# Optimization experiments

Measured on AMD Instinct MI355X. Metric: run time of the kernel, lower is better.

The kernel has to match this reference:

```python
import jax, jax.numpy as jnp
import numpy as np

B, N, C = 32, 128, 128
HE = 64                      # n_hidden_edge
FILTERS = [64, 256, 512]
K = 3
NREL = 2
NH = 256                     # n_hidden
OUT = 10
EPS_BN = 1e-5


def _lin(key, fin, fout):
    return jax.random.normal(key, (fin, fout), jnp.float32) / np.sqrt(fin)


def setup_inputs() -> dict:
    key = jax.random.key(0)
    ks = iter(jax.random.split(key, 64))
    x = jax.random.normal(next(ks), (B, N, C), jnp.float32)
    # ragged mask: first n_b nodes active
    n_nodes = jax.random.randint(next(ks), (B,), 64, N + 1)
    mask = (jnp.arange(N)[None, :] < n_nodes[:, None]).astype(jnp.float32)
    A = jax.random.uniform(next(ks), (B, N, N), jnp.float32)
    A = A * mask[:, :, None] * mask[:, None, :]
    inp = {"x": x, "A": A, "mask": mask}
    # edge predictor MLP: Linear(2C,HE) -> ReLU -> Linear(HE,1)
    inp["eW1"] = _lin(next(ks), 2 * C, HE)
    inp["eb1"] = jnp.zeros((HE,), jnp.float32)
    inp["eW2"] = _lin(next(ks), HE, 1)
    inp["eb2"] = jnp.zeros((1,), jnp.float32)
    # 3 GraphConv layers: fc (in*K*NREL -> f), BN eval params
    fin = C
    for li, f in enumerate(FILTERS):
        inp[f"gW{li}"] = _lin(next(ks), fin * K * NREL, f)
        inp[f"gb{li}"] = jnp.zeros((f,), jnp.float32)
        inp[f"g{li}g"] = jnp.ones((f,), jnp.float32)
        inp[f"g{li}b"] = jnp.zeros((f,), jnp.float32)
        inp[f"g{li}m"] = 0.1 * jax.random.normal(next(ks), (f,), jnp.float32)
        inp[f"g{li}v"] = jax.random.uniform(next(ks), (f,), jnp.float32) + 0.5
        fin = f
    # classifier fc (dropout is identity in eval)
    inp["fW1"] = _lin(next(ks), FILTERS[-1], NH)
    inp["fb1"] = jnp.zeros((NH,), jnp.float32)
    inp["fW2"] = _lin(next(ks), NH, OUT)
    inp["fb2"] = jnp.zeros((OUT,), jnp.float32)
    return inp


def _edge_adjacency(x, mask, eW1, eb1, eW2, eb2):
    # edge_pred(cat(x_i,x_j)) for all pairs; flipped pass == transpose of scores
    u = x @ eW1[:C]          # [B,N,HE] (contribution of node i slot)
    v = x @ eW1[C:]          # [B,N,HE] (contribution of node j slot)
    h = jax.nn.relu(u[:, :, None, :] + v[:, None, :, :] + eb1)   # [B,N,N,HE]
    s = jnp.einsum('bijh,h->bij', h, eW2[:, 0]) + eb2[0]          # [B,N,N]
    y = jnp.exp(0.5 * (s + jnp.swapaxes(s, 1, 2)))
    # only masked upper-triangular pairs (i<j) were scattered in the original
    tri = jnp.triu(jnp.ones((N, N), bool), 1)
    pm = tri[None, :, :] * (mask[:, :, None] * mask[:, None, :])
    A_pred = y * pm
    rs = jnp.sum(A_pred, axis=2)                                 # row sums (torch sum over dim 1 of [N,N])
    rs = jnp.where(rs == 0.0, 1.0, rs)
    An = A_pred / rs[:, :, None]
    return An + jnp.swapaxes(An, 1, 2)


def _gconv(xh, A2, mask, W, b, g, be, m, v):
    outs = []
    for rel in range(A2.shape[-1]):
        Ar = A2[..., rel]
        # K>=2, scale_identity=False -> no identity added
        D = (jnp.sum(Ar, axis=1) + 1e-5) ** (-0.5)               # [B,N]
        L = D[:, :, None] * Ar * D[:, None, :]
        Xt = [xh, jnp.matmul(L, xh)]
        for _ in range(2, K):
            Xt.append(2.0 * jnp.matmul(L, Xt[-1]) - Xt[-2])
        outs.append(jnp.concatenate(Xt, axis=2))
    h = jnp.concatenate(outs, axis=2) @ W + b
    h = h * mask[:, :, None]
    h = (h - m) / jnp.sqrt(v + EPS_BN) * g + be                  # BatchNorm1d eval over channel dim
    return jax.nn.relu(h)


def reference(x, A, mask, eW1, eb1, eW2, eb2,
              gW0, gb0, g0g, g0b, g0m, g0v,
              gW1, gb1, g1g, g1b, g1m, g1v,
              gW2, gb2, g2g, g2b, g2m, g2v,
              fW1, fb1, fW2, fb2):
    An = _edge_adjacency(x, mask, eW1, eb1, eW2, eb2)
    A2 = jnp.stack((A, An), axis=3)                              # [B,N,N,2]
    h = _gconv(x, A2, mask, gW0, gb0, g0g, g0b, g0m, g0v)
    h = _gconv(h, A2, mask, gW1, gb1, g1g, g1b, g1m, g1v)
    h = _gconv(h, A2, mask, gW2, gb2, g2g, g2b, g2m, g2v)
    pooled = jnp.max(h, axis=1)                                  # [B, 512]
    # fc: Dropout(eval=id) -> Linear -> Dropout(eval=id) -> Linear (no activation)
    return (pooled @ fW1 + fb1) @ fW2 + fb2
```

## Files before the change

kernel.cpp:

```cpp
#include <hip/hip_runtime.h>

#define Bk 32
#define Nn 128
#define Cc 128
#define HE 64
#define BN_EPS 1e-5f

typedef __attribute__((ext_vector_type(8))) short short8;
typedef __attribute__((ext_vector_type(4))) float floatx4;

#define OFF_UV   ((size_t)0)
#define OFF_AP   ((size_t)524288)
#define OFF_LB   ((size_t)1048576)
#define OFF_H0   ((size_t)1572864)
#define OFF_H1   ((size_t)1835008)
#define OFF_WC   ((size_t)2899968)
#define OFF_BC   ((size_t)2905088)
#define OFF_XB0  ((size_t)2905104)
#define OFF_XB   ((size_t)3167248)
#define OFF_WT   ((size_t)6312976)
#define WUV_OFS  933888

__device__ __forceinline__ unsigned short f2b(float f) {
    unsigned int x = __float_as_uint(f);
    unsigned int r = x + 0x7FFFu + ((x >> 16) & 1u);
    return (unsigned short)(r >> 16);
}

__global__ __launch_bounds__(256) void prep_all(const float* __restrict__ W0,
                                                const float* __restrict__ W1,
                                                const float* __restrict__ W2,
                                                const float* __restrict__ eW1,
                                                const float* __restrict__ fW1,
                                                const float* __restrict__ fb1,
                                                const float* __restrict__ fW2,
                                                const float* __restrict__ fb2,
                                                const float* __restrict__ x,
                                                unsigned short* __restrict__ Wt,
                                                float* __restrict__ Wc,
                                                float* __restrict__ bc,
                                                unsigned short* __restrict__ xb0) {
    __shared__ unsigned short Ts[64][65];
    int bid = blockIdx.x, tid = threadIdx.x;
    if (bid < 228) {
        const float* src; unsigned short* dst; int N, ldK, k0, n0;
        if (bid < 12)      { src = W0; dst = Wt;          N = 64;  ldK = 768;  k0 = bid * 64;        n0 = 0; }
        else if (bid < 36) { int t = bid - 12; src = W1; dst = Wt + 49152;  N = 256; ldK = 384;  k0 = (t % 6) * 64;  n0 = (t / 6) * 64; }
        else               { int t = bid - 36; src = W2; dst = Wt + 147456; N = 512; ldK = 1536; k0 = (t % 24) * 64; n0 = (t / 24) * 64; }
#pragma unroll
        for (int p = 0; p < 16; ++p) {
            int e = tid + p * 256; int r = e >> 6, c = e & 63;
            Ts[r][c] = f2b(src[(size_t)(k0 + r) * N + n0 + c]);
        }
        __syncthreads();
#pragma unroll
        for (int p = 0; p < 16; ++p) {
            int e = tid + p * 256; int n = e >> 6, k = e & 63;
            dst[(size_t)(n0 + n) * ldK + k0 + k] = Ts[k][n];
        }
        return;
    }
    if (bid < 232) {
        int tt = bid - 228;
        int half = tt >> 1, kt = tt & 1;
        int k0 = kt * 64;
        unsigned short* Wuv = Wt + WUV_OFS;
#pragma unroll
        for (int p = 0; p < 16; ++p) {
            int e = tid + p * 256; int r = e >> 6, c = e & 63;
            Ts[r][c] = f2b(eW1[(size_t)(half * 128 + k0 + r) * 64 + c]);
        }
        __syncthreads();
#pragma unroll
        for (int p = 0; p < 16; ++p) {
            int e = tid + p * 256; int n = e >> 6, k = e & 63;
            Wuv[(size_t)(half * 64 + n) * 128 + k0 + k] = Ts[k][n];
        }
        return;
    }
    if (bid < 253) {
        int e = (bid - 232) * 256 + tid;
        if (e < 5120) {
            int i = e / 10, j = e - i * 10;
            float acc = 0.f;
            for (int h = 0; h < 256; ++h) acc += fW1[(size_t)i * 256 + h] * fW2[(size_t)h * 10 + j];
            Wc[e] = acc;
        } else if (e < 5130) {
            int j = e - 5120;
            float acc = fb2[j];
            for (int h = 0; h < 256; ++h) acc += fb1[h] * fW2[(size_t)h * 10 + j];
            bc[j] = acc;
        }
        return;
    }
    {
        int idx = (bid - 253) * 256 + tid;
        float4 vv = ((const float4*)x)[idx];
        ushort4 o;
        o.x = f2b(vv.x); o.y = f2b(vv.y); o.z = f2b(vv.z); o.w = f2b(vv.w);
        ((ushort4*)xb0)[idx] = o;
    }
}

__global__ __launch_bounds__(256) void uv_mfma(const unsigned short* __restrict__ xb0,
                                               const unsigned short* __restrict__ Wuv,
                                               const float* __restrict__ eb1,
                                               float* __restrict__ uv) {
    __shared__ __align__(16) unsigned short As[128 * 40];
    __shared__ __align__(16) unsigned short Bs[64 * 40];
    int tid = threadIdx.x;
    int w = tid >> 6, lane = tid & 63, quad = lane >> 4, lr = lane & 15;
    int row0 = blockIdx.y * 128, col0 = blockIdx.x * 64;
    floatx4 acc[2][4];
#pragma unroll
    for (int rt = 0; rt < 2; ++rt)
#pragma unroll
        for (int ct = 0; ct < 4; ++ct) acc[rt][ct] = (floatx4){0.f, 0.f, 0.f, 0.f};
    int arow[2], asub[2];
#pragma unroll
    for (int i = 0; i < 2; ++i) { int ch = tid + i * 256; arow[i] = ch >> 2; asub[i] = ch & 3; }
    int brow = tid >> 2, bsub = tid & 3;
    for (int k0 = 0; k0 < 128; k0 += 32) {
        short8 ra[2];
#pragma unroll
        for (int i = 0; i < 2; ++i)
            ra[i] = *(const short8*)(xb0 + (size_t)(row0 + arow[i]) * 128 + k0 + asub[i] * 8);
        short8 rb = *(const short8*)(Wuv + (size_t)(col0 + brow) * 128 + k0 + bsub * 8);
        __syncthreads();
#pragma unroll
        for (int i = 0; i < 2; ++i) *(short8*)&As[arow[i] * 40 + asub[i] * 8] = ra[i];
        *(short8*)&Bs[brow * 40 + bsub * 8] = rb;
        __syncthreads();
        short8 a[2], b[4];
#pragma unroll
        for (int rt = 0; rt < 2; ++rt)
            a[rt] = *(const short8*)&As[(w * 32 + rt * 16 + lr) * 40 + quad * 8];
#pragma unroll
        for (int ct = 0; ct < 4; ++ct)
            b[ct] = *(const short8*)&Bs[(ct * 16 + lr) * 40 + quad * 8];
#pragma unroll
        for (int rt = 0; rt < 2; ++rt)
#pragma unroll
            for (int ct = 0; ct < 4; ++ct)
                acc[rt][ct] = __builtin_amdgcn_mfma_f32_16x16x32_bf16(a[rt], b[ct], acc[rt][ct], 0, 0, 0);
    }
#pragma unroll
    for (int rt = 0; rt < 2; ++rt) {
        int rbase = row0 + w * 32 + rt * 16 + quad * 4;
#pragma unroll
        for (int ct = 0; ct < 4; ++ct) {
            int col = col0 + ct * 16 + lr;
            float bi = (col < 64) ? eb1[col] : 0.f;
#pragma unroll
            for (int reg = 0; reg < 4; ++reg)
                uv[(size_t)(rbase + reg) * 128 + col] = acc[rt][ct][reg] + bi;
        }
    }
}

__global__ __launch_bounds__(256) void edge_sym(const float* __restrict__ uv,
                                                const float* __restrict__ eW2,
                                                const float* __restrict__ eb2,
                                                const float* __restrict__ mask,
                                                float* __restrict__ ap) {
    __shared__ __align__(16) float ui[16][68], vi[16][68], uj[16][68], vj[16][68];
    __shared__ __align__(16) float w2[64];
    int t = blockIdx.x, b = blockIdx.y;
    int ti = 0, rem = t;
    for (;;) { int w = 8 - ti; if (rem < w) break; rem -= w; ++ti; }
    int tj = ti + rem;
    int i0 = ti * 16, j0 = tj * 16;
    int tid = threadIdx.x;
    int r = tid >> 4, c4 = (tid & 15) * 4;
    const float* uvb = uv + (size_t)b * Nn * 128;
    *(float4*)&ui[r][c4] = *(const float4*)(uvb + (size_t)(i0 + r) * 128 + c4);
    *(float4*)&vi[r][c4] = *(const float4*)(uvb + (size_t)(i0 + r) * 128 + 64 + c4);
    *(float4*)&uj[r][c4] = *(const float4*)(uvb + (size_t)(j0 + r) * 128 + c4);
    *(float4*)&vj[r][c4] = *(const float4*)(uvb + (size_t)(j0 + r) * 128 + 64 + c4);
    if (tid < 64) w2[tid] = eW2[tid];
    __syncthreads();
    int il = tid >> 4, jl = tid & 15;
    int gi = i0 + il, gj = j0 + jl;
    if (gj <= gi) return;
    float d = 0.f;
#pragma unroll
    for (int h4 = 0; h4 < 16; ++h4) {
        float4 a1 = *(const float4*)&ui[il][h4 * 4];
        float4 b1 = *(const float4*)&vj[jl][h4 * 4];
        float4 a2 = *(const float4*)&uj[jl][h4 * 4];
        float4 b2 = *(const float4*)&vi[il][h4 * 4];
        float4 ww = *(const float4*)&w2[h4 * 4];
        d += (fmaxf(a1.x + b1.x, 0.f) + fmaxf(a2.x + b2.x, 0.f)) * ww.x
           + (fmaxf(a1.y + b1.y, 0.f) + fmaxf(a2.y + b2.y, 0.f)) * ww.y
           + (fmaxf(a1.z + b1.z, 0.f) + fmaxf(a2.z + b2.z, 0.f)) * ww.z
           + (fmaxf(a1.w + b1.w, 0.f) + fmaxf(a2.w + b2.w, 0.f)) * ww.w;
    }
    float p = 0.5f * d + eb2[0];
    float mi = mask[b * Nn + gi], mj = mask[b * Nn + gj];
    float val = (mi != 0.f && mj != 0.f) ? expf(fminf(p, 80.f)) : 0.f;
    ap[((size_t)(b * Nn + gi)) * Nn + gj] = val;
}

__global__ __launch_bounds__(256) void adj_L(const float* __restrict__ ap,
                                             const float* __restrict__ A,
                                             unsigned short* __restrict__ Lb) {
    int bid = blockIdx.x, tid = threadIdx.x;
    if (bid < 32) {
        int b = bid;
        __shared__ float apS[128][129];
        __shared__ float part[256], invS[128], t1S[128], Dv[128];
        const float* apg = ap + (size_t)b * Nn * Nn;
        for (int k = 0; k < 64; ++k) {
            int idx = tid + k * 256;
            int i = idx >> 7, j = idx & 127;
            float g = apg[idx];
            apS[i][j] = (j > i) ? g : 0.f;
        }
        __syncthreads();
        {
            int row = tid >> 1, half = tid & 1;
            float s0 = 0.f;
            for (int j = half * 64; j < half * 64 + 64; ++j) s0 += apS[row][j];
            part[tid] = s0;
        }
        __syncthreads();
        if (tid < 128) {
            float rsum = part[tid * 2] + part[tid * 2 + 1];
            invS[tid] = (rsum == 0.f) ? 1.f : (1.f / rsum);
            t1S[tid]  = (rsum == 0.f) ? 0.f : 1.f;
        }
        __syncthreads();
        {
            int col = tid >> 1, half = tid & 1;
            float s0 = 0.f;
            for (int j = half * 64; j < half * 64 + 64; ++j) s0 += apS[j][col] * invS[j];
            part[tid] = s0;
        }
        __syncthreads();
        if (tid < 128) Dv[tid] = rsqrtf(t1S[tid] + part[tid * 2] + part[tid * 2 + 1] + 1e-5f);
        __syncthreads();
        unsigned short* Lo = Lb + ((size_t)(Bk + b)) * Nn * Nn;
        for (int k = 0; k < 64; ++k) {
            int idx = tid + k * 256;
            int i = idx >> 7, j = idx & 127;
            float an = apS[i][j] * invS[i] + apS[j][i] * invS[j];
            Lo[idx] = f2b(Dv[i] * an * Dv[j]);
        }
    } else {
        int b = bid - 32;
        const float* Ar = A + (size_t)b * Nn * Nn;
        __shared__ float part2[256];
        __shared__ float Ds[128];
        int j = tid & 127, half = tid >> 7;
        float sum = 0.f;
        for (int i = half * 64; i < half * 64 + 64; ++i) sum += Ar[i * Nn + j];
        part2[tid] = sum;
        __syncthreads();
        if (tid < 128) Ds[tid] = rsqrtf(part2[tid] + part2[tid + 128] + 1e-5f);
        __syncthreads();
        unsigned short* Lo = Lb + (size_t)b * Nn * Nn;
        for (int k = 0; k < 64; ++k) {
            int idx = tid + k * 256;
            int i = idx >> 7, jj = idx & 127;
            Lo[idx] = f2b(Ds[i] * Ar[idx] * Ds[jj]);
        }
    }
}

template <int FIN>
__global__ __launch_bounds__(256) void cheb_v4(const unsigned short* __restrict__ Lb,
                                               const float* __restrict__ xin,
                                               unsigned short* __restrict__ Xb) {
    constexpr int LDK = 136;
    __shared__ __align__(16) unsigned short XsT[32 * LDK];
    __shared__ __align__(16) unsigned short T1T[32 * LDK];
    int z = blockIdx.y;
    int b = z & 31, rel = z >> 5;
    int c0 = blockIdx.x * 32;
    int tid = threadIdx.x;
    int w = tid >> 6, lane = tid & 63, quad = lane >> 4, lr = lane & 15;
    const unsigned short* Lp = Lb + ((size_t)(rel * Bk + b)) * Nn * Nn;
    const float* Xp = xin + (size_t)b * Nn * FIN;
    const int ld6 = 6 * FIN;
    unsigned short* Xo = Xb + (size_t)b * Nn * ld6 + rel * 3 * FIN;

    short8 aL[2][4];
#pragma unroll
    for (int rt = 0; rt < 2; ++rt) {
        int row = w * 32 + rt * 16 + lr;
#pragma unroll
        for (int kc = 0; kc < 4; ++kc)
            aL[rt][kc] = *(const short8*)(Lp + (size_t)row * Nn + kc * 32 + quad * 8);
    }
    {
        int node = tid >> 1, cb = (tid & 1) * 16;
        const float* xr = Xp + (size_t)node * FIN + c0 + cb;
        unsigned short* t0w = Xo + (size_t)node * ld6 + c0 + cb;
#pragma unroll
        for (int i = 0; i < 4; ++i) {
            float4 vv = *(const float4*)(xr + i * 4);
            ushort4 o;
            o.x = f2b(vv.x); o.y = f2b(vv.y); o.z = f2b(vv.z); o.w = f2b(vv.w);
            *(ushort4*)(t0w + i * 4) = o;
            XsT[(cb + i * 4 + 0) * LDK + node] = o.x;
            XsT[(cb + i * 4 + 1) * LDK + node] = o.y;
            XsT[(cb + i * 4 + 2) * LDK + node] = o.z;
            XsT[(cb + i * 4 + 3) * LDK + node] = o.w;
        }
    }
    __syncthreads();

    floatx4 acc1[2][2];
#pragma unroll
    for (int rt = 0; rt < 2; ++rt)
#pragma unroll
        for (int ct = 0; ct < 2; ++ct) acc1[rt][ct] = (floatx4){0.f, 0.f, 0.f, 0.f};
#pragma unroll
    for (int kc = 0; kc < 4; ++kc) {
        short8 bb[2];
#pragma unroll
        for (int ct = 0; ct < 2; ++ct)
            bb[ct] = *(const short8*)&XsT[(ct * 16 + lr) * LDK + kc * 32 + quad * 8];
#pragma unroll
        for (int rt = 0; rt < 2; ++rt)
#pragma unroll
            for (int ct = 0; ct < 2; ++ct)
                acc1[rt][ct] = __builtin_amdgcn_mfma_f32_16x16x32_bf16(aL[rt][kc], bb[ct], acc1[rt][ct], 0, 0, 0);
    }
#pragma unroll
    for (int rt = 0; rt < 2; ++rt) {
        int rb = (w * 2 + rt) * 16 + quad * 4;
#pragma unroll
        for (int ct = 0; ct < 2; ++ct) {
            int col = ct * 16 + lr;
            ushort4 o;
            o.x = f2b(acc1[rt][ct][0]); o.y = f2b(acc1[rt][ct][1]);
            o.z = f2b(acc1[rt][ct][2]); o.w = f2b(acc1[rt][ct][3]);
            *(ushort4*)&T1T[col * LDK + rb] = o;
        }
    }
    __syncthreads();

    {
        int node = tid >> 1, cb = (tid & 1) * 16;
        unsigned short* t1w = Xo + (size_t)node * ld6 + FIN + c0 + cb;
#pragma unroll
        for (int i = 0; i < 4; ++i) {
            ushort4 o;
            o.x = T1T[(cb + i * 4 + 0) * LDK + node];
            o.y = T1T[(cb + i * 4 + 1) * LDK + node];
            o.z = T1T[(cb + i * 4 + 2) * LDK + node];
            o.w = T1T[(cb + i * 4 + 3) * LDK + node];
            *(ushort4*)(t1w + i * 4) = o;
        }
    }
    floatx4 acc2[2][2];
#pragma unroll
    for (int rt = 0; rt < 2; ++rt)
#pragma unroll
        for (int ct = 0; ct < 2; ++ct) acc2[rt][ct] = (floatx4){0.f, 0.f, 0.f, 0.f};
#pragma unroll
    for (int kc = 0; kc < 4; ++kc) {
        short8 bb[2];
#pragma unroll
        for (int ct = 0; ct < 2; ++ct)
            bb[ct] = *(const short8*)&T1T[(ct * 16 + lr) * LDK + kc * 32 + quad * 8];
#pragma unroll
        for (int rt = 0; rt < 2; ++rt)
#pragma unroll
            for (int ct = 0; ct < 2; ++ct)
                acc2[rt][ct] = __builtin_amdgcn_mfma_f32_16x16x32_bf16(aL[rt][kc], bb[ct], acc2[rt][ct], 0, 0, 0);
    }
#pragma unroll
    for (int rt = 0; rt < 2; ++rt) {
        int rb = (w * 2 + rt) * 16 + quad * 4;
#pragma unroll
        for (int ct = 0; ct < 2; ++ct) {
            int col = ct * 16 + lr;
            ushort4 o;
            float t0a = Xp[(size_t)(rb + 0) * FIN + c0 + col];
            float t0b = Xp[(size_t)(rb + 1) * FIN + c0 + col];
            float t0c = Xp[(size_t)(rb + 2) * FIN + c0 + col];
            float t0d = Xp[(size_t)(rb + 3) * FIN + c0 + col];
            o.x = f2b(2.f * acc2[rt][ct][0] - t0a);
            o.y = f2b(2.f * acc2[rt][ct][1] - t0b);
            o.z = f2b(2.f * acc2[rt][ct][2] - t0c);
            o.w = f2b(2.f * acc2[rt][ct][3] - t0d);
            *(ushort4*)&XsT[col * LDK + rb] = o;
        }
    }
    __syncthreads();
    {
        int node = tid >> 1, cb = (tid & 1) * 16;
        unsigned short* t2w = Xo + (size_t)node * ld6 + 2 * FIN + c0 + cb;
#pragma unroll
        for (int i = 0; i < 4; ++i) {
            ushort4 o;
            o.x = XsT[(cb + i * 4 + 0) * LDK + node];
            o.y = XsT[(cb + i * 4 + 1) * LDK + node];
            o.z = XsT[(cb + i * 4 + 2) * LDK + node];
            o.w = XsT[(cb + i * 4 + 3) * LDK + node];
            *(ushort4*)(t2w + i * 4) = o;
        }
    }
}

template <int RT, bool POOL>
__global__ __launch_bounds__(256) void fc_mfma(const unsigned short* __restrict__ Xb,
                                               const unsigned short* __restrict__ Wt,
                                               const float* __restrict__ bias,
                                               const float* __restrict__ mask,
                                               const float* __restrict__ bnG,
                                               const float* __restrict__ bnB,
                                               const float* __restrict__ bnM,
                                               const float* __restrict__ bnV,
                                               float* __restrict__ out,
                                               const float* __restrict__ Wc,
                                               const float* __restrict__ bc,
                                               float* __restrict__ outc,
                                               int Kd, int F) {
    __shared__ __align__(16) unsigned short As[RT * 64 * 40];
    __shared__ __align__(16) unsigned short Bs[64 * 40];
    __shared__ float wmax[4][64];
    int tid = threadIdx.x;
    int w = tid >> 6, lane = tid & 63, quad = lane >> 4, lr = lane & 15;
    int row0 = blockIdx.y * (RT * 64), col0 = blockIdx.x * 64;

    floatx4 acc[RT][4];
#pragma unroll
    for (int rt = 0; rt < RT; ++rt)
#pragma unroll
        for (int ct = 0; ct < 4; ++ct) acc[rt][ct] = (floatx4){0.f, 0.f, 0.f, 0.f};

    int arow[RT], asub[RT];
#pragma unroll
    for (int i = 0; i < RT; ++i) { int ch = tid + i * 256; arow[i] = ch >> 2; asub[i] = ch & 3; }
    int brow = tid >> 2, bsub = tid & 3;

    for (int k0 = 0; k0 < Kd; k0 += 32) {
        short8 ra[RT];
#pragma unroll
        for (int i = 0; i < RT; ++i)
            ra[i] = *(const short8*)(Xb + (size_t)(row0 + arow[i]) * Kd + k0 + asub[i] * 8);
        short8 rb = *(const short8*)(Wt + (size_t)(col0 + brow) * Kd + k0 + bsub * 8);
        __syncthreads();
#pragma unroll
        for (int i = 0; i < RT; ++i)
            *(short8*)&As[arow[i] * 40 + asub[i] * 8] = ra[i];
        *(short8*)&Bs[brow * 40 + bsub * 8] = rb;
        __syncthreads();
        short8 a[RT], b[4];
#pragma unroll
        for (int rt = 0; rt < RT; ++rt)
            a[rt] = *(const short8*)&As[(w * RT * 16 + rt * 16 + lr) * 40 + quad * 8];
#pragma unroll
        for (int ct = 0; ct < 4; ++ct)
            b[ct] = *(const short8*)&Bs[(ct * 16 + lr) * 40 + quad * 8];
#pragma unroll
        for (int rt = 0; rt < RT; ++rt)
#pragma unroll
            for (int ct = 0; ct < 4; ++ct)
                acc[rt][ct] = __builtin_amdgcn_mfma_f32_16x16x32_bf16(a[rt], b[ct], acc[rt][ct], 0, 0, 0);
    }

    float cm[4] = {0.f, 0.f, 0.f, 0.f};
#pragma unroll
    for (int rt = 0; rt < RT; ++rt) {
        int rbase = row0 + w * RT * 16 + rt * 16 + quad * 4;
#pragma unroll
        for (int ct = 0; ct < 4; ++ct) {
            int col = col0 + ct * 16 + lr;
            float bi = bias[col];
            float sc = rsqrtf(bnV[col] + BN_EPS) * bnG[col];
            float bm = bnM[col], bb = bnB[col];
#pragma unroll
            for (int reg = 0; reg < 4; ++reg) {
                int row = rbase + reg;
                float h = acc[rt][ct][reg] + bi;
                h *= mask[row];
                h = (h - bm) * sc + bb;
                h = fmaxf(h, 0.f);
                if (POOL) cm[ct] = fmaxf(cm[ct], h);
                else      out[(size_t)row * F + col] = h;
            }
        }
    }
    if (POOL) {
#pragma unroll
        for (int ct = 0; ct < 4; ++ct) {
            cm[ct] = fmaxf(cm[ct], __shfl_xor(cm[ct], 16));
            cm[ct] = fmaxf(cm[ct], __shfl_xor(cm[ct], 32));
            if (quad == 0) wmax[w][ct * 16 + lr] = cm[ct];
        }
        __syncthreads();
        if (tid < 64) {
            float g = fmaxf(fmaxf(wmax[0][tid], wmax[1][tid]), fmaxf(wmax[2][tid], wmax[3][tid]));
            float s[10];
#pragma unroll
            for (int o = 0; o < 10; ++o) s[o] = g * Wc[(size_t)(col0 + tid) * 10 + o];
#pragma unroll
            for (int ofs = 32; ofs > 0; ofs >>= 1)
#pragma unroll
                for (int o = 0; o < 10; ++o) s[o] += __shfl_down(s[o], ofs);
            if (tid == 0) {
                int b = blockIdx.y;
#pragma unroll
                for (int o = 0; o < 10; ++o) {
                    float v = s[o] + ((blockIdx.x == 0) ? bc[o] : 0.f);
                    atomicAdd(&outc[b * 10 + o], v);
                }
            }
        }
    }
}

extern "C" void kernel_launch(void* const* d_in, const int* in_sizes, int n_in,
                              void* d_out, int out_size, void* d_ws, size_t ws_size,
                              hipStream_t stream) {
    const float* x    = (const float*)d_in[0];
    const float* Ain  = (const float*)d_in[1];
    const float* mask = (const float*)d_in[2];
    const float* eW1  = (const float*)d_in[3];
    const float* eb1  = (const float*)d_in[4];
    const float* eW2  = (const float*)d_in[5];
    const float* eb2  = (const float*)d_in[6];
    const float* fW1  = (const float*)d_in[25];
    const float* fb1  = (const float*)d_in[26];
    const float* fW2  = (const float*)d_in[27];
    const float* fb2  = (const float*)d_in[28];

    float* ws = (float*)d_ws;
    float* uv = ws + OFF_UV;
    float* ap = ws + OFF_AP;
    unsigned short* Lb = (unsigned short*)(ws + OFF_LB);
    float* h0 = ws + OFF_H0;
    float* h1 = ws + OFF_H1;
    float* Wc = ws + OFF_WC;
    float* bc = ws + OFF_BC;
    unsigned short* xb0 = (unsigned short*)(ws + OFF_XB0);
    unsigned short* Xb  = (unsigned short*)(ws + OFF_XB);
    unsigned short* Wt  = (unsigned short*)(ws + OFF_WT);

    hipMemsetAsync(d_out, 0, (size_t)out_size * sizeof(float), stream);

    prep_all<<<765, 256, 0, stream>>>((const float*)d_in[7], (const float*)d_in[13],
                                      (const float*)d_in[19], eW1, fW1, fb1, fW2, fb2, x,
                                      Wt, Wc, bc, xb0);

    uv_mfma<<<dim3(2, 32), 256, 0, stream>>>(xb0, Wt + WUV_OFS, eb1, uv);
    edge_sym<<<dim3(36, Bk), 256, 0, stream>>>(uv, eW2, eb2, mask, ap);
    adj_L<<<64, 256, 0, stream>>>(ap, Ain, Lb);

    const float* xins[3] = {x, h0, h1};
    const unsigned short* Wts[3] = {Wt, Wt + 49152, Wt + 147456};
    const int Kds[3] = {768, 384, 1536};
    for (int li = 0; li < 3; ++li) {
        int base = 7 + li * 6;
        const float* gb = (const float*)d_in[base + 1];
        const float* gg = (const float*)d_in[base + 2];
        const float* gB = (const float*)d_in[base + 3];
        const float* gm = (const float*)d_in[base + 4];
        const float* gv = (const float*)d_in[base + 5];

        if (li == 0)      cheb_v4<128><<<dim3(4, 64), 256, 0, stream>>>(Lb, xins[li], Xb);
        else if (li == 1) cheb_v4<64><<<dim3(2, 64), 256, 0, stream>>>(Lb, xins[li], Xb);
        else              cheb_v4<256><<<dim3(8, 64), 256, 0, stream>>>(Lb, xins[li], Xb);

        if (li == 0)
            fc_mfma<1, false><<<dim3(1, 64), 256, 0, stream>>>(
                Xb, Wts[li], gb, mask, gg, gB, gm, gv, h0, nullptr, nullptr, nullptr, Kds[li], 64);
        else if (li == 1)
            fc_mfma<2, false><<<dim3(4, 32), 256, 0, stream>>>(
                Xb, Wts[li], gb, mask, gg, gB, gm, gv, h1, nullptr, nullptr, nullptr, Kds[li], 256);
        else
            fc_mfma<2, true><<<dim3(8, 32), 256, 0, stream>>>(
                Xb, Wts[li], gb, mask, gg, gB, gm, gv, nullptr, Wc, bc, (float*)d_out, Kds[li], 512);
    }
}
```

Before: 235.1 us.

## Fuse all stages into one persistent kernel with grid-wide barriers

Replaces the sequence of separate kernel launches (prep, uv, edge, adjacency, three cheb+fc layers) with a single persistent kernel of 512 blocks that loops over virtual blocks per stage. Stages are separated by a software grid barrier built on global atomics. Independent work is co-scheduled within a stage, such as the A-side adjacency with uv and the first cheb pass with the edge scoring. The adjacency-normalisation stage is split so the A branch runs early, and ap is zeroed in the prep stage. This removes per-launch overhead and tail gaps but adds barrier spin cost. It also depends on all 512 blocks being co-resident, with no cooperative launch guaranteeing that.

```diff
diff --git a/kernel.cpp b/kernel.cpp
--- a/kernel.cpp
+++ b/kernel.cpp
@@ -3,8 +3,8 @@
 #define Bk 32
 #define Nn 128
 #define Cc 128
-#define HE 64
 #define BN_EPS 1e-5f
+#define GRIDN 512
 
 typedef __attribute__((ext_vector_type(8))) short short8;
 typedef __attribute__((ext_vector_type(4))) float floatx4;
@@ -27,90 +27,120 @@
     return (unsigned short)(r >> 16);
 }
 
-__global__ __launch_bounds__(256) void prep_all(const float* __restrict__ W0,
-                                                const float* __restrict__ W1,
-                                                const float* __restrict__ W2,
-                                                const float* __restrict__ eW1,
-                                                const float* __restrict__ fW1,
-                                                const float* __restrict__ fb1,
-                                                const float* __restrict__ fW2,
-                                                const float* __restrict__ fb2,
-                                                const float* __restrict__ x,
-                                                unsigned short* __restrict__ Wt,
-                                                float* __restrict__ Wc,
-                                                float* __restrict__ bc,
-                                                unsigned short* __restrict__ xb0) {
-    __shared__ unsigned short Ts[64][65];
-    int bid = blockIdx.x, tid = threadIdx.x;
-    if (bid < 228) {
+union __align__(16) SMem {
+    struct { unsigned short Ts[64][65]; } prep;
+    struct { unsigned short As[128 * 40]; unsigned short Bs[64 * 40]; } uv;
+    struct { float ui[16][68]; float vi[16][68];
+             float uj[16][68]; float vj[16][68]; float w2[64]; } edge;
+    struct { float part[256]; float invS[128]; float t1S[128]; float Dv[128]; } adj;
+    struct { unsigned short XsT[32 * 136]; unsigned short T1T[32 * 136]; } cheb;
+    struct { unsigned short As[2 * 64 * 40]; unsigned short Bs[64 * 40];
+             float wmax[4][64]; } fc;
+};
+
+__device__ unsigned g_cnt = 0;
+__device__ unsigned g_gen = 0;
+
+__device__ __forceinline__ void gsync() {
+    __syncthreads();
+    if (threadIdx.x == 0) {
+        __threadfence();
+        unsigned gen = __hip_atomic_load(&g_gen, __ATOMIC_RELAXED, __HIP_MEMORY_SCOPE_AGENT);
+        unsigned arr = __hip_atomic_fetch_add(&g_cnt, 1u, __ATOMIC_ACQ_REL, __HIP_MEMORY_SCOPE_AGENT) + 1u;
+        if (arr == (unsigned)GRIDN) {
+            __hip_atomic_store(&g_cnt, 0u, __ATOMIC_RELAXED, __HIP_MEMORY_SCOPE_AGENT);
+            __hip_atomic_fetch_add(&g_gen, 1u, __ATOMIC_ACQ_REL, __HIP_MEMORY_SCOPE_AGENT);
+        } else {
+            while (__hip_atomic_load(&g_gen, __ATOMIC_RELAXED, __HIP_MEMORY_SCOPE_AGENT) == gen)
+                __builtin_amdgcn_s_sleep(2);
+        }
+        __threadfence();
+    }
+    __syncthreads();
+}
+
+struct MArgs {
+    const float *x, *A, *mask, *eW1, *eb1, *eW2, *eb2;
+    const float *W0, *W1, *W2;
+    const float *gb0, *gg0, *gB0, *gm0, *gv0;
+    const float *gb1, *gg1, *gB1, *gm1, *gv1;
+    const float *gb2, *gg2, *gB2, *gm2, *gv2;
+    const float *fW1, *fb1, *fW2, *fb2;
+    float *uv, *ap, *h0, *h1, *Wc, *bc;
+    unsigned short *Lb, *xb0, *Xb, *Wt;
+    float *outc;
+};
+
+__device__ __forceinline__ void st_prep(SMem& sm, int vb, int tid, const MArgs& a) {
+    if (vb < 228) {
         const float* src; unsigned short* dst; int N, ldK, k0, n0;
-        if (bid < 12)      { src = W0; dst = Wt;          N = 64;  ldK = 768;  k0 = bid * 64;        n0 = 0; }
-        else if (bid < 36) { int t = bid - 12; src = W1; dst = Wt + 49152;  N = 256; ldK = 384;  k0 = (t % 6) * 64;  n0 = (t / 6) * 64; }
-        else               { int t = bid - 36; src = W2; dst = Wt + 147456; N = 512; ldK = 1536; k0 = (t % 24) * 64; n0 = (t / 24) * 64; }
+        if (vb < 12)      { src = a.W0; dst = a.Wt;          N = 64;  ldK = 768;  k0 = vb * 64;       n0 = 0; }
+        else if (vb < 36) { int t = vb - 12; src = a.W1; dst = a.Wt + 49152;  N = 256; ldK = 384;  k0 = (t % 6) * 64;  n0 = (t / 6) * 64; }
+        else              { int t = vb - 36; src = a.W2; dst = a.Wt + 147456; N = 512; ldK = 1536; k0 = (t % 24) * 64; n0 = (t / 24) * 64; }
 #pragma unroll
         for (int p = 0; p < 16; ++p) {
             int e = tid + p * 256; int r = e >> 6, c = e & 63;
-            Ts[r][c] = f2b(src[(size_t)(k0 + r) * N + n0 + c]);
+            sm.prep.Ts[r][c] = f2b(src[(size_t)(k0 + r) * N + n0 + c]);
         }
         __syncthreads();
 #pragma unroll
         for (int p = 0; p < 16; ++p) {
             int e = tid + p * 256; int n = e >> 6, k = e & 63;
-            dst[(size_t)(n0 + n) * ldK + k0 + k] = Ts[k][n];
-        }
-        return;
-    }
-    if (bid < 232) {
-        int tt = bid - 228;
+            dst[(size_t)(n0 + n) * ldK + k0 + k] = sm.prep.Ts[k][n];
+        }
+    } else if (vb < 232) {
+        int tt = vb - 228;
         int half = tt >> 1, kt = tt & 1;
         int k0 = kt * 64;
-        unsigned short* Wuv = Wt + WUV_OFS;
+        unsigned short* Wuv = a.Wt + WUV_OFS;
 #pragma unroll
         for (int p = 0; p < 16; ++p) {
             int e = tid + p * 256; int r = e >> 6, c = e & 63;
-            Ts[r][c] = f2b(eW1[(size_t)(half * 128 + k0 + r) * 64 + c]);
+            sm.prep.Ts[r][c] = f2b(a.eW1[(size_t)(half * 128 + k0 + r) * 64 + c]);
         }
         __syncthreads();
 #pragma unroll
         for (int p = 0; p < 16; ++p) {
             int e = tid + p * 256; int n = e >> 6, k = e & 63;
-            Wuv[(size_t)(half * 64 + n) * 128 + k0 + k] = Ts[k][n];
-        }
-        return;
-    }
-    if (bid < 253) {
-        int e = (bid - 232) * 256 + tid;
+            Wuv[(size_t)(half * 64 + n) * 128 + k0 + k] = sm.prep.Ts[k][n];
+        }
+    } else if (vb < 253) {
+        int e = (vb - 232) * 256 + tid;
         if (e < 5120) {
             int i = e / 10, j = e - i * 10;
             float acc = 0.f;
-            for (int h = 0; h < 256; ++h) acc += fW1[(size_t)i * 256 + h] * fW2[(size_t)h * 10 + j];
-            Wc[e] = acc;
+            for (int h = 0; h < 256; ++h) acc += a.fW1[(size_t)i * 256 + h] * a.fW2[(size_t)h * 10 + j];
+            a.Wc[e] = acc;
         } else if (e < 5130) {
             int j = e - 5120;
-            float acc = fb2[j];
-            for (int h = 0; h < 256; ++h) acc += fb1[h] * fW2[(size_t)h * 10 + j];
-            bc[j] = acc;
-        }
-        return;
-    }
-    {
-        int idx = (bid - 253) * 256 + tid;
-        float4 vv = ((const float4*)x)[idx];
+            float acc = a.fb2[j];
+            for (int h = 0; h < 256; ++h) acc += a.fb1[h] * a.fW2[(size_t)h * 10 + j];
+            a.bc[j] = acc;
+        }
+    } else if (vb < 765) {
+        int idx = (vb - 253) * 256 + tid;
+        float4 vv = ((const float4*)a.x)[idx];
         ushort4 o;
         o.x = f2b(vv.x); o.y = f2b(vv.y); o.z = f2b(vv.z); o.w = f2b(vv.w);
-        ((ushort4*)xb0)[idx] = o;
-    }
-}
-
-__global__ __launch_bounds__(256) void uv_mfma(const unsigned short* __restrict__ xb0,
-                                               const unsigned short* __restrict__ Wuv,
-                                               const float* __restrict__ eb1,
-                                               float* __restrict__ uv) {
-    __shared__ __align__(16) unsigned short As[128 * 40];
-    __shared__ __align__(16) unsigned short Bs[64 * 40];
-    int tid = threadIdx.x;
+        ((ushort4*)a.xb0)[idx] = o;
+    } else {
+        int b = vb - 765;
+        float4* dst = (float4*)(a.ap + (size_t)b * Nn * Nn);
+        float4 z4 = {0.f, 0.f, 0.f, 0.f};
+#pragma unroll
+        for (int i = 0; i < 16; ++i) dst[tid + i * 256] = z4;
+    }
+}
+
+__device__ __forceinline__ void st_uv(SMem& sm, int tid, int bx, int by,
+                                      const unsigned short* __restrict__ xb0,
+                                      const unsigned short* __restrict__ Wuv,
+                                      const float* __restrict__ eb1,
+                                      float* __restrict__ uv) {
+    unsigned short* As = sm.uv.As;
+    unsigned short* Bs = sm.uv.Bs;
     int w = tid >> 6, lane = tid & 63, quad = lane >> 4, lr = lane & 15;
-    int row0 = blockIdx.y * 128, col0 = blockIdx.x * 64;
+    int row0 = by * 128, col0 = bx * 64;
     floatx4 acc[2][4];
 #pragma unroll
     for (int rt = 0; rt < 2; ++rt)
@@ -131,18 +161,18 @@
         for (int i = 0; i < 2; ++i) *(short8*)&As[arow[i] * 40 + asub[i] * 8] = ra[i];
         *(short8*)&Bs[brow * 40 + bsub * 8] = rb;
         __syncthreads();
-        short8 a[2], b[4];
+        short8 av[2], bv[4];
 #pragma unroll
         for (int rt = 0; rt < 2; ++rt)
-            a[rt] = *(const short8*)&As[(w * 32 + rt * 16 + lr) * 40 + quad * 8];
+            av[rt] = *(const short8*)&As[(w * 32 + rt * 16 + lr) * 40 + quad * 8];
 #pragma unroll
         for (int ct = 0; ct < 4; ++ct)
-            b[ct] = *(const short8*)&Bs[(ct * 16 + lr) * 40 + quad * 8];
+            bv[ct] = *(const short8*)&Bs[(ct * 16 + lr) * 40 + quad * 8];
 #pragma unroll
         for (int rt = 0; rt < 2; ++rt)
 #pragma unroll
             for (int ct = 0; ct < 4; ++ct)
-                acc[rt][ct] = __builtin_amdgcn_mfma_f32_16x16x32_bf16(a[rt], b[ct], acc[rt][ct], 0, 0, 0);
+                acc[rt][ct] = __builtin_amdgcn_mfma_f32_16x16x32_bf16(av[rt], bv[ct], acc[rt][ct], 0, 0, 0);
     }
 #pragma unroll
     for (int rt = 0; rt < 2; ++rt) {
@@ -158,126 +188,117 @@
     }
 }
 
-__global__ __launch_bounds__(256) void edge_sym(const float* __restrict__ uv,
-                                                const float* __restrict__ eW2,
-                                                const float* __restrict__ eb2,
-                                                const float* __restrict__ mask,
-                                                float* __restrict__ ap) {
-    __shared__ __align__(16) float ui[16][68], vi[16][68], uj[16][68], vj[16][68];
-    __shared__ __align__(16) float w2[64];
-    int t = blockIdx.x, b = blockIdx.y;
+__device__ __forceinline__ void st_adjA(SMem& sm, int tid, int b,
+                                        const float* __restrict__ A,
+                                        unsigned short* __restrict__ Lb) {
+    const float* Ar = A + (size_t)b * Nn * Nn;
+    int j = tid & 127, half = tid >> 7;
+    float sum = 0.f;
+    for (int i = half * 64; i < half * 64 + 64; ++i) sum += Ar[i * Nn + j];
+    sm.adj.part[tid] = sum;
+    __syncthreads();
+    if (tid < 128) sm.adj.Dv[tid] = rsqrtf(sm.adj.part[tid] + sm.adj.part[tid + 128] + 1e-5f);
+    __syncthreads();
+    unsigned short* Lo = Lb + (size_t)b * Nn * Nn;
+    for (int k = 0; k < 64; ++k) {
+        int idx = tid + k * 256;
+        int i = idx >> 7, jj = idx & 127;
+        Lo[idx] = f2b(sm.adj.Dv[i] * Ar[idx] * sm.adj.Dv[jj]);
+    }
+}
+
+__device__ __forceinline__ void st_edge(SMem& sm, int tid, int t, int b,
+                                        const float* __restrict__ uv,
+                                        const float* __restrict__ eW2,
+                                        const float* __restrict__ eb2,
+                                        const float* __restrict__ mask,
+                                        float* __restrict__ ap) {
     int ti = 0, rem = t;
     for (;;) { int w = 8 - ti; if (rem < w) break; rem -= w; ++ti; }
     int tj = ti + rem;
     int i0 = ti * 16, j0 = tj * 16;
-    int tid = threadIdx.x;
     int r = tid >> 4, c4 = (tid & 15) * 4;
     const float* uvb = uv + (size_t)b * Nn * 128;
-    *(float4*)&ui[r][c4] = *(const float4*)(uvb + (size_t)(i0 + r) * 128 + c4);
-    *(float4*)&vi[r][c4] = *(const float4*)(uvb + (size_t)(i0 + r) * 128 + 64 + c4);
-    *(float4*)&uj[r][c4] = *(const float4*)(uvb + (size_t)(j0 + r) * 128 + c4);
-    *(float4*)&vj[r][c4] = *(const float4*)(uvb + (size_t)(j0 + r) * 128 + 64 + c4);
-    if (tid < 64) w2[tid] = eW2[tid];
+    *(float4*)&sm.edge.ui[r][c4] = *(const float4*)(uvb + (size_t)(i0 + r) * 128 + c4);
+    *(float4*)&sm.edge.vi[r][c4] = *(const float4*)(uvb + (size_t)(i0 + r) * 128 + 64 + c4);
+    *(float4*)&sm.edge.uj[r][c4] = *(const float4*)(uvb + (size_t)(j0 + r) * 128 + c4);
+    *(float4*)&sm.edge.vj[r][c4] = *(const float4*)(uvb + (size_t)(j0 + r) * 128 + 64 + c4);
+    if (tid < 64) sm.edge.w2[tid] = eW2[tid];
     __syncthreads();
     int il = tid >> 4, jl = tid & 15;
     int gi = i0 + il, gj = j0 + jl;
-    if (gj <= gi) return;
-    float d = 0.f;
-#pragma unroll
-    for (int h4 = 0; h4 < 16; ++h4) {
-        float4 a1 = *(const float4*)&ui[il][h4 * 4];
-        float4 b1 = *(const float4*)&vj[jl][h4 * 4];
-        float4 a2 = *(const float4*)&uj[jl][h4 * 4];
-        float4 b2 = *(const float4*)&vi[il][h4 * 4];
-        float4 ww = *(const float4*)&w2[h4 * 4];
-        d += (fmaxf(a1.x + b1.x, 0.f) + fmaxf(a2.x + b2.x, 0.f)) * ww.x
-           + (fmaxf(a1.y + b1.y, 0.f) + fmaxf(a2.y + b2.y, 0.f)) * ww.y
-           + (fmaxf(a1.z + b1.z, 0.f) + fmaxf(a2.z + b2.z, 0.f)) * ww.z
-           + (fmaxf(a1.w + b1.w, 0.f) + fmaxf(a2.w + b2.w, 0.f)) * ww.w;
-    }
-    float p = 0.5f * d + eb2[0];
-    float mi = mask[b * Nn + gi], mj = mask[b * Nn + gj];
-    float val = (mi != 0.f && mj != 0.f) ? expf(fminf(p, 80.f)) : 0.f;
-    ap[((size_t)(b * Nn + gi)) * Nn + gj] = val;
-}
-
-__global__ __launch_bounds__(256) void adj_L(const float* __restrict__ ap,
-                                             const float* __restrict__ A,
-                                             unsigned short* __restrict__ Lb) {
-    int bid = blockIdx.x, tid = threadIdx.x;
-    if (bid < 32) {
-        int b = bid;
-        __shared__ float apS[128][129];
-        __shared__ float part[256], invS[128], t1S[128], Dv[128];
-        const float* apg = ap + (size_t)b * Nn * Nn;
-        for (int k = 0; k < 64; ++k) {
-            int idx = tid + k * 256;
-            int i = idx >> 7, j = idx & 127;
-            float g = apg[idx];
-            apS[i][j] = (j > i) ? g : 0.f;
-        }
-        __syncthreads();
-        {
-            int row = tid >> 1, half = tid & 1;
-            float s0 = 0.f;
-            for (int j = half * 64; j < half * 64 + 64; ++j) s0 += apS[row][j];
-            part[tid] = s0;
-        }
-        __syncthreads();
-        if (tid < 128) {
-            float rsum = part[tid * 2] + part[tid * 2 + 1];
-            invS[tid] = (rsum == 0.f) ? 1.f : (1.f / rsum);
-            t1S[tid]  = (rsum == 0.f) ? 0.f : 1.f;
-        }
-        __syncthreads();
-        {
-            int col = tid >> 1, half = tid & 1;
-            float s0 = 0.f;
-            for (int j = half * 64; j < half * 64 + 64; ++j) s0 += apS[j][col] * invS[j];
-            part[tid] = s0;
-        }
-        __syncthreads();
-        if (tid < 128) Dv[tid] = rsqrtf(t1S[tid] + part[tid * 2] + part[tid * 2 + 1] + 1e-5f);
-        __syncthreads();
-        unsigned short* Lo = Lb + ((size_t)(Bk + b)) * Nn * Nn;
-        for (int k = 0; k < 64; ++k) {
-            int idx = tid + k * 256;
-            int i = idx >> 7, j = idx & 127;
-            float an = apS[i][j] * invS[i] + apS[j][i] * invS[j];
-            Lo[idx] = f2b(Dv[i] * an * Dv[j]);
-        }
-    } else {
-        int b = bid - 32;
-        const float* Ar = A + (size_t)b * Nn * Nn;
-        __shared__ float part2[256];
-        __shared__ float Ds[128];
-        int j = tid & 127, half = tid >> 7;
-        float sum = 0.f;
-        for (int i = half * 64; i < half * 64 + 64; ++i) sum += Ar[i * Nn + j];
-        part2[tid] = sum;
-        __syncthreads();
-        if (tid < 128) Ds[tid] = rsqrtf(part2[tid] + part2[tid + 128] + 1e-5f);
-        __syncthreads();
-        unsigned short* Lo = Lb + (size_t)b * Nn * Nn;
-        for (int k = 0; k < 64; ++k) {
-            int idx = tid + k * 256;
-            int i = idx >> 7, jj = idx & 127;
-            Lo[idx] = f2b(Ds[i] * Ar[idx] * Ds[jj]);
-        }
+    if (gj > gi) {
+        float d = 0.f;
+#pragma unroll
+        for (int h4 = 0; h4 < 16; ++h4) {
+            float4 a1 = *(const float4*)&sm.edge.ui[il][h4 * 4];
+            float4 b1 = *(const float4*)&sm.edge.vj[jl][h4 * 4];
+            float4 a2 = *(const float4*)&sm.edge.uj[jl][h4 * 4];
+            float4 b2 = *(const float4*)&sm.edge.vi[il][h4 * 4];
+            float4 ww = *(const float4*)&sm.edge.w2[h4 * 4];
+            d += (fmaxf(a1.x + b1.x, 0.f) + fmaxf(a2.x + b2.x, 0.f)) * ww.x
+               + (fmaxf(a1.y + b1.y, 0.f) + fmaxf(a2.y + b2.y, 0.f)) * ww.y
+               + (fmaxf(a1.z + b1.z, 0.f) + fmaxf(a2.z + b2.z, 0.f)) * ww.z
+               + (fmaxf(a1.w + b1.w, 0.f) + fmaxf(a2.w + b2.w, 0.f)) * ww.w;
+        }
+        float p = 0.5f * d + eb2[0];
+        float mi = mask[b * Nn + gi], mj = mask[b * Nn + gj];
+        float val = (mi != 0.f && mj != 0.f) ? expf(fminf(p, 80.f)) : 0.f;
+        ap[((size_t)(b * Nn + gi)) * Nn + gj] = val;
+    }
+}
+
+__device__ __forceinline__ void st_adjAn(SMem& sm, int tid, int b,
+                                         const float* __restrict__ ap,
+                                         unsigned short* __restrict__ Lb) {
+    const float* apg = ap + (size_t)b * Nn * Nn;
+    {
+        int row = tid >> 1, half = tid & 1;
+        const float* rp = apg + (size_t)row * Nn + half * 64;
+        float s0 = 0.f;
+        for (int jj = 0; jj < 64; jj += 4) {
+            float4 v = *(const float4*)(rp + jj);
+            s0 += v.x; s0 += v.y; s0 += v.z; s0 += v.w;
+        }
+        sm.adj.part[tid] = s0;
+    }
+    __syncthreads();
+    if (tid < 128) {
+        float rsum = sm.adj.part[tid * 2] + sm.adj.part[tid * 2 + 1];
+        sm.adj.invS[tid] = (rsum == 0.f) ? 1.f : (1.f / rsum);
+        sm.adj.t1S[tid]  = (rsum == 0.f) ? 0.f : 1.f;
+    }
+    __syncthreads();
+    {
+        int col = tid >> 1, half = tid & 1;
+        float s0 = 0.f;
+        for (int jj = half * 64; jj < half * 64 + 64; ++jj)
+            s0 += apg[(size_t)jj * Nn + col] * sm.adj.invS[jj];
+        sm.adj.part[tid] = s0;
+    }
+    __syncthreads();
+    if (tid < 128)
+        sm.adj.Dv[tid] = rsqrtf(sm.adj.t1S[tid] + sm.adj.part[tid * 2] + sm.adj.part[tid * 2 + 1] + 1e-5f);
+    __syncthreads();
+    unsigned short* Lo = Lb + ((size_t)(Bk + b)) * Nn * Nn;
+    for (int k = 0; k < 64; ++k) {
+        int idx = tid + k * 256;
+        int i = idx >> 7, j = idx & 127;
+        float an = apg[idx] * sm.adj.invS[i] + apg[(size_t)j * Nn + i] * sm.adj.invS[j];
+        Lo[idx] = f2b(sm.adj.Dv[i] * an * sm.adj.Dv[j]);
     }
 }
 
 template <int FIN>
-__global__ __launch_bounds__(256) void cheb_v4(const unsigned short* __restrict__ Lb,
-                                               const float* __restrict__ xin,
-                                               unsigned short* __restrict__ Xb) {
+__device__ __forceinline__ void st_cheb(SMem& sm, int tid, int c0blk, int z,
+                                        const unsigned short* __restrict__ Lb,
+                                        const float* __restrict__ xin,
+                                        unsigned short* __restrict__ Xb) {
     constexpr int LDK = 136;
-    __shared__ __align__(16) unsigned short XsT[32 * LDK];
-    __shared__ __align__(16) unsigned short T1T[32 * LDK];
-    int z = blockIdx.y;
+    unsigned short* XsT = sm.cheb.XsT;
+    unsigned short* T1T = sm.cheb.T1T;
     int b = z & 31, rel = z >> 5;
-    int c0 = blockIdx.x * 32;
-    int tid = threadIdx.x;
+    int c0 = c0blk * 32;
     int w = tid >> 6, lane = tid & 63, quad = lane >> 4, lr = lane & 15;
     const unsigned short* Lp = Lb + ((size_t)(rel * Bk + b)) * Nn * Nn;
     const float* Xp = xin + (size_t)b * Nn * FIN;
@@ -406,25 +427,24 @@
 }
 
 template <int RT, bool POOL>
-__global__ __launch_bounds__(256) void fc_mfma(const unsigned short* __restrict__ Xb,
-                                               const unsigned short* __restrict__ Wt,
-                                               const float* __restrict__ bias,
-                                               const float* __restrict__ mask,
-                                               const float* __restrict__ bnG,
-                                               const float* __restrict__ bnB,
-                                               const float* __restrict__ bnM,
-                                               const float* __restrict__ bnV,
-                                               float* __restrict__ out,
-                                               const float* __restrict__ Wc,
-                                               const float* __restrict__ bc,
-                                               float* __restrict__ outc,
-                                               int Kd, int F) {
-    __shared__ __align__(16) unsigned short As[RT * 64 * 40];
-    __shared__ __align__(16) unsigned short Bs[64 * 40];
-    __shared__ float wmax[4][64];
-    int tid = threadIdx.x;
+__device__ __forceinline__ void st_fc(SMem& sm, int tid, int bx, int by,
+                                      const unsigned short* __restrict__ Xb,
+                                      const unsigned short* __restrict__ Wt,
+                                      const float* __restrict__ bias,
+                                      const float* __restrict__ mask,
+                                      const float* __restrict__ bnG,
+                                      const float* __restrict__ bnB,
+                                      const float* __restrict__ bnM,
+                                      const float* __restrict__ bnV,
+                                      float* __restrict__ out,
+                                      const float* __restrict__ Wc,
+                                      const float* __restrict__ bc,
+                                      float* __restrict__ outc,
+                                      int Kd, int F) {
+    unsigned short* As = sm.fc.As;
+    unsigned short* Bs = sm.fc.Bs;
     int w = tid >> 6, lane = tid & 63, quad = lane >> 4, lr = lane & 15;
-    int row0 = blockIdx.y * (RT * 64), col0 = blockIdx.x * 64;
+    int row0 = by * (RT * 64), col0 = bx * 64;
 
     floatx4 acc[RT][4];
 #pragma unroll
@@ -449,18 +469,18 @@
             *(short8*)&As[arow[i] * 40 + asub[i] * 8] = ra[i];
         *(short8*)&Bs[brow * 40 + bsub * 8] = rb;
         __syncthreads();
-        short8 a[RT], b[4];
+        short8 av[RT], bv[4];
 #pragma unroll
         for (int rt = 0; rt < RT; ++rt)
-            a[rt] = *(const short8*)&As[(w * RT * 16 + rt * 16 + lr) * 40 + quad * 8];
+            av[rt] = *(const short8*)&As[(w * RT * 16 + rt * 16 + lr) * 40 + quad * 8];
 #pragma unroll
         for (int ct = 0; ct < 4; ++ct)
-            b[ct] = *(const short8*)&Bs[(ct * 16 + lr) * 40 + quad * 8];
+            bv[ct] = *(const short8*)&Bs[(ct * 16 + lr) * 40 + quad * 8];
 #pragma unroll
         for (int rt = 0; rt < RT; ++rt)
 #pragma unroll
             for (int ct = 0; ct < 4; ++ct)
-                acc[rt][ct] = __builtin_amdgcn_mfma_f32_16x16x32_bf16(a[rt], b[ct], acc[rt][ct], 0, 0, 0);
+                acc[rt][ct] = __builtin_amdgcn_mfma_f32_16x16x32_bf16(av[rt], bv[ct], acc[rt][ct], 0, 0, 0);
     }
 
     float cm[4] = {0.f, 0.f, 0.f, 0.f};
@@ -490,11 +510,12 @@
         for (int ct = 0; ct < 4; ++ct) {
             cm[ct] = fmaxf(cm[ct], __shfl_xor(cm[ct], 16));
             cm[ct] = fmaxf(cm[ct], __shfl_xor(cm[ct], 32));
-            if (quad == 0) wmax[w][ct * 16 + lr] = cm[ct];
+            if (quad == 0) sm.fc.wmax[w][ct * 16 + lr] = cm[ct];
         }
         __syncthreads();
         if (tid < 64) {
-            float g = fmaxf(fmaxf(wmax[0][tid], wmax[1][tid]), fmaxf(wmax[2][tid], wmax[3][tid]));
+            float g = fmaxf(fmaxf(sm.fc.wmax[0][tid], sm.fc.wmax[1][tid]),
+                            fmaxf(sm.fc.wmax[2][tid], sm.fc.wmax[3][tid]));
             float s[10];
 #pragma unroll
             for (int o = 0; o < 10; ++o) s[o] = g * Wc[(size_t)(col0 + tid) * 10 + o];
@@ -503,77 +524,99 @@
 #pragma unroll
                 for (int o = 0; o < 10; ++o) s[o] += __shfl_down(s[o], ofs);
             if (tid == 0) {
-                int b = blockIdx.y;
 #pragma unroll
                 for (int o = 0; o < 10; ++o) {
-                    float v = s[o] + ((blockIdx.x == 0) ? bc[o] : 0.f);
-                    atomicAdd(&outc[b * 10 + o], v);
+                    float v = s[o] + ((bx == 0) ? bc[o] : 0.f);
+                    atomicAdd(&outc[by * 10 + o], v);
                 }
             }
         }
+    }
+}
+
+__global__ __launch_bounds__(256, 2) void mega(MArgs a) {
+    __shared__ SMem sm;
+    int tid = threadIdx.x, bid = blockIdx.x;
+
+    for (int vb = bid; vb < 797; vb += GRIDN) { st_prep(sm, vb, tid, a); __syncthreads(); }
+    gsync();
+    for (int vb = bid; vb < 96; vb += GRIDN) {
+        if (vb < 64) st_uv(sm, tid, vb & 1, vb >> 1, a.xb0, a.Wt + WUV_OFS, a.eb1, a.uv);
+        else         st_adjA(sm, tid, vb - 64, a.A, a.Lb);
+        __syncthreads();
+    }
+    gsync();
+    for (int vb = bid; vb < 1280; vb += GRIDN) {
+        if (vb < 1152) st_edge(sm, tid, vb % 36, vb / 36, a.uv, a.eW2, a.eb2, a.mask, a.ap);
+        else { int v = vb - 1152; st_cheb<128>(sm, tid, v & 3, v >> 2, a.Lb, a.x, a.Xb); }
+        __syncthreads();
+    }
+    gsync();
+    for (int vb = bid; vb < 32; vb += GRIDN) { st_adjAn(sm, tid, vb, a.ap, a.Lb); __syncthreads(); }
+    gsync();
+    for (int vb = bid; vb < 128; vb += GRIDN) { st_cheb<128>(sm, tid, vb & 3, 32 + (vb >> 2), a.Lb, a.x, a.Xb); __syncthreads(); }
+    gsync();
+    for (int vb = bid; vb < 64; vb += GRIDN) {
+        st_fc<1, false>(sm, tid, 0, vb, a.Xb, a.Wt, a.gb0, a.mask, a.gg0, a.gB0, a.gm0, a.gv0,
+                        a.h0, nullptr, nullptr, nullptr, 768, 64);
+        __syncthreads();
+    }
+    gsync();
+    for (int vb = bid; vb < 128; vb += GRIDN) { st_cheb<64>(sm, tid, vb & 1, vb >> 1, a.Lb, a.h0, a.Xb); __syncthreads(); }
+    gsync();
+    for (int vb = bid; vb < 128; vb += GRIDN) {
+        st_fc<2, false>(sm, tid, vb & 3, vb >> 2, a.Xb, a.Wt + 49152, a.gb1, a.mask, a.gg1, a.gB1, a.gm1, a.gv1,
+                        a.h1, nullptr, nullptr, nullptr, 384, 256);
+        __syncthreads();
+    }
+    gsync();
+    for (int vb = bid; vb < 512; vb += GRIDN) { st_cheb<256>(sm, tid, vb & 7, vb >> 3, a.Lb, a.h1, a.Xb); __syncthreads(); }
+    gsync();
+    for (int vb = bid; vb < 256; vb += GRIDN) {
+        st_fc<2, true>(sm, tid, vb & 7, vb >> 3, a.Xb, a.Wt + 147456, a.gb2, a.mask, a.gg2, a.gB2, a.gm2, a.gv2,
+                       nullptr, a.Wc, a.bc, a.outc, 1536, 512);
+        __syncthreads();
     }
 }
 
 extern "C" void kernel_launch(void* const* d_in, const int* in_sizes, int n_in,
                               void* d_out, int out_size, void* d_ws, size_t ws_size,
                               hipStream_t stream) {
-    const float* x    = (const float*)d_in[0];
-    const float* Ain  = (const float*)d_in[1];
-    const float* mask = (const float*)d_in[2];
-    const float* eW1  = (const float*)d_in[3];
-    const float* eb1  = (const float*)d_in[4];
-    const float* eW2  = (const float*)d_in[5];
-    const float* eb2  = (const float*)d_in[6];
-    const float* fW1  = (const float*)d_in[25];
-    const float* fb1  = (const float*)d_in[26];
-    const float* fW2  = (const float*)d_in[27];
-    const float* fb2  = (const float*)d_in[28];
-
+    (void)in_sizes; (void)n_in; (void)ws_size;
     float* ws = (float*)d_ws;
-    float* uv = ws + OFF_UV;
-    float* ap = ws + OFF_AP;
-    unsigned short* Lb = (unsigned short*)(ws + OFF_LB);
-    float* h0 = ws + OFF_H0;
-    float* h1 = ws + OFF_H1;
-    float* Wc = ws + OFF_WC;
-    float* bc = ws + OFF_BC;
-    unsigned short* xb0 = (unsigned short*)(ws + OFF_XB0);
-    unsigned short* Xb  = (unsigned short*)(ws + OFF_XB);
-    unsigned short* Wt  = (unsigned short*)(ws + OFF_WT);
+
+    MArgs a;
+    a.x    = (const float*)d_in[0];
+    a.A    = (const float*)d_in[1];
+    a.mask = (const float*)d_in[2];
+    a.eW1  = (const float*)d_in[3];
+    a.eb1  = (const float*)d_in[4];
+    a.eW2  = (const float*)d_in[5];
+    a.eb2  = (const float*)d_in[6];
+    a.W0   = (const float*)d_in[7];
+    a.gb0  = (const float*)d_in[8];  a.gg0 = (const float*)d_in[9];  a.gB0 = (const float*)d_in[10];
+    a.gm0  = (const float*)d_in[11]; a.gv0 = (const float*)d_in[12];
+    a.W1   = (const float*)d_in[13];
+    a.gb1  = (const float*)d_in[14]; a.gg1 = (const float*)d_in[15]; a.gB1 = (const float*)d_in[16];
+    a.gm1  = (const float*)d_in[17]; a.gv1 = (const float*)d_in[18];
+    a.W2   = (const float*)d_in[19];
+    a.gb2  = (const float*)d_in[20]; a.gg2 = (const float*)d_in[21]; a.gB2 = (const float*)d_in[22];
+    a.gm2  = (const float*)d_in[23]; a.gv2 = (const float*)d_in[24];
+    a.fW1  = (const float*)d_in[25]; a.fb1 = (const float*)d_in[26];
+    a.fW2  = (const float*)d_in[27]; a.fb2 = (const float*)d_in[28];
+
+    a.uv  = ws + OFF_UV;
+    a.ap  = ws + OFF_AP;
+    a.h0  = ws + OFF_H0;
+    a.h1  = ws + OFF_H1;
+    a.Wc  = ws + OFF_WC;
+    a.bc  = ws + OFF_BC;
+    a.Lb  = (unsigned short*)(ws + OFF_LB);
+    a.xb0 = (unsigned short*)(ws + OFF_XB0);
+    a.Xb  = (unsigned short*)(ws + OFF_XB);
+    a.Wt  = (unsigned short*)(ws + OFF_WT);
+    a.outc = (float*)d_out;
 
     hipMemsetAsync(d_out, 0, (size_t)out_size * sizeof(float), stream);
-
-    prep_all<<<765, 256, 0, stream>>>((const float*)d_in[7], (const float*)d_in[13],
-                                      (const float*)d_in[19], eW1, fW1, fb1, fW2, fb2, x,
-                                      Wt, Wc, bc, xb0);
-
-    uv_mfma<<<dim3(2, 32), 256, 0, stream>>>(xb0, Wt + WUV_OFS, eb1, uv);
-    edge_sym<<<dim3(36, Bk), 256, 0, stream>>>(uv, eW2, eb2, mask, ap);
-    adj_L<<<64, 256, 0, stream>>>(ap, Ain, Lb);
-
-    const float* xins[3] = {x, h0, h1};
-    const unsigned short* Wts[3] = {Wt, Wt + 49152, Wt + 147456};
-    const int Kds[3] = {768, 384, 1536};
-    for (int li = 0; li < 3; ++li) {
-        int base = 7 + li * 6;
-        const float* gb = (const float*)d_in[base + 1];
-        const float* gg = (const float*)d_in[base + 2];
-        const float* gB = (const float*)d_in[base + 3];
-        const float* gm = (const float*)d_in[base + 4];
-        const float* gv = (const float*)d_in[base + 5];
-
-        if (li == 0)      cheb_v4<128><<<dim3(4, 64), 256, 0, stream>>>(Lb, xins[li], Xb);
-        else if (li == 1) cheb_v4<64><<<dim3(2, 64), 256, 0, stream>>>(Lb, xins[li], Xb);
-        else              cheb_v4<256><<<dim3(8, 64), 256, 0, stream>>>(Lb, xins[li], Xb);
-
-        if (li == 0)
-            fc_mfma<1, false><<<dim3(1, 64), 256, 0, stream>>>(
-                Xb, Wts[li], gb, mask, gg, gB, gm, gv, h0, nullptr, nullptr, nullptr, Kds[li], 64);
-        else if (li == 1)
-            fc_mfma<2, false><<<dim3(4, 32), 256, 0, stream>>>(
-                Xb, Wts[li], gb, mask, gg, gB, gm, gv, h1, nullptr, nullptr, nullptr, Kds[li], 256);
-        else
-            fc_mfma<2, true><<<dim3(8, 32), 256, 0, stream>>>(
-                Xb, Wts[li], gb, mask, gg, gB, gm, gv, nullptr, Wc, bc, (float*)d_out, Kds[li], 512);
-    }
-}
+    mega<<<GRIDN, 256, 0, stream>>>(a);
+}
```

Measured after the change: 793.9 us. 3.38x slower.
